# Performance work log

Hardware: AMD Instinct MI355X
Metric: run time of the kernel (lower is better)

The kernel has to match this reference:

```python
import jax, jax.numpy as jnp
import numpy as np
import math

B, T, C, V = 64, 4096, 3, 16
HEADS = 4
ROT_HIDDEN = 128
MLP_HIDDEN = 256
NUM_CLASSES = 12
BLOCK_SIZES = (16, 32, 64)
IN_FEAT = C * V  # 48
FEAT_DIM = HEADS * 7 * len(BLOCK_SIZES)  # 84


def _linear_params(key, fan_in, fan_out):
    kw, kb = jax.random.split(key)
    lim = 1.0 / np.sqrt(fan_in)
    w = jax.random.uniform(kw, (fan_in, fan_out), jnp.float32, -lim, lim)
    b = jax.random.uniform(kb, (fan_out,), jnp.float32, -lim, lim)
    return w, b


def setup_inputs() -> dict:
    key = jax.random.key(0)
    ks = jax.random.split(key, 7)
    x = jax.random.normal(ks[0], (B, T, C, V), jnp.float32)
    w1, b1 = _linear_params(ks[1], IN_FEAT, ROT_HIDDEN)
    w2, b2 = _linear_params(ks[2], ROT_HIDDEN, ROT_HIDDEN)
    w3, b3 = _linear_params(ks[3], ROT_HIDDEN, HEADS * 4)
    p1, pb1 = _linear_params(ks[4], FEAT_DIM, MLP_HIDDEN)
    p2, pb2 = _linear_params(ks[5], MLP_HIDDEN, MLP_HIDDEN)
    p3, pb3 = _linear_params(ks[6], MLP_HIDDEN, NUM_CLASSES)
    return dict(x=x, w1=w1, b1=b1, w2=w2, b2=b2, w3=w3, b3=b3,
                p1=p1, pb1=pb1, p2=p2, pb2=pb2, p3=p3, pb3=pb3)


def _extract_tsf(rot, bs):
    # rot: (B, H, T, F). Non-overlapping blocks of size bs (T % bs == 0).
    b, h, t, f = rot.shape
    n = t // bs
    z = rot.reshape(b, h, n, bs, f)
    mean = z.mean(axis=3)
    m2 = (z * z).mean(axis=3)
    std = jnp.sqrt(((z - mean[:, :, :, None, :]) ** 2).mean(axis=3))
    z_min = z.min(axis=3)
    z_max = z.max(axis=3)
    rms = jnp.sqrt(m2 + 1e-8)
    mac = jnp.abs(z[:, :, :, 1:, :] - z[:, :, :, :-1, :]).mean(axis=3)
    energy = m2  # (z**2).sum / bs == mean of squares
    feat = jnp.stack([mean, std, z_min, z_max, rms, mac, energy], axis=-1)  # (B,H,n,F,7)
    # mean over blocks (n) then over channels (F) -> (B, H, 7)
    return feat.mean(axis=2).mean(axis=2)


def reference(x, w1, b1, w2, b2, w3, b3, p1, pb1, p2, pb2, p3, pb3):
    b, t, c, v = x.shape
    xf = x.reshape(b, t, c * v)
    f = xf.shape[-1]
    pad = (3 - f % 3) % 3
    if pad > 0:
        xf = jnp.pad(xf, ((0, 0), (0, 0), (0, pad)))
    g = xf.shape[-1] // 3
    x_xyz = xf.reshape(b, t, g, 3)

    # rotation-parameter MLP (dropout is identity in eval mode)
    gf = xf.mean(axis=1)[:, :IN_FEAT]
    h1 = jax.nn.relu(gf @ w1 + b1)
    h2 = jax.nn.relu(h1 @ w2 + b2)
    rot = jnp.tanh(h2 @ w3 + b3).reshape(b, HEADS, 4)
    axis = rot[..., :3]
    axis = axis / (jnp.linalg.norm(axis, axis=-1, keepdims=True) + 1e-8)
    theta = rot[..., 3] * math.pi  # (B, H)

    # Rodrigues rotation: v (B,1,T,g,3), k (B,H,1,1,3)
    vvec = x_xyz[:, None]
    k = axis[:, :, None, None, :]
    th = theta[:, :, None, None, None]
    cos_t, sin_t = jnp.cos(th), jnp.sin(th)
    cross = jnp.cross(jnp.broadcast_to(k, (b, HEADS, t, g, 3)),
                      jnp.broadcast_to(vvec, (b, HEADS, t, g, 3)), axis=-1)
    dot = (k * vvec).sum(axis=-1, keepdims=True)
    rotated = vvec * cos_t + cross * sin_t + k * dot * (1.0 - cos_t)  # (B,H,T,g,3)
    rotated = rotated.reshape(b, HEADS, t, g * 3)

    # block-wise stats: per head, per block size, 7 stats -> (B, H, nbs, 7)
    feats = jnp.stack([_extract_tsf(rotated, bs) for bs in BLOCK_SIZES], axis=2)
    feat = feats.reshape(b, HEADS * len(BLOCK_SIZES) * 7)  # (B, 84)

    q1 = jax.nn.relu(feat @ p1 + pb1)
    q2 = jax.nn.relu(q1 @ p2 + pb2)
    return q2 @ p3 + pb3
```

## Files before the change

kernel.cpp:

```cpp
#include <hip/hip_runtime.h>
#include <math.h>


#define PI_F 3.14159265358979323846f

__global__ __launch_bounds__(384) void k_colmean(const float4* __restrict__ x4,
                                                 float* __restrict__ gfpart) {
    int b = blockIdx.x >> 3;
    int chunk = blockIdx.x & 7;
    int tid = threadIdx.x;
    int j4 = tid % 12, r = tid / 12;
    const float4* p = x4 + ((size_t)(b * 4096 + chunk * 512 + r)) * 12 + j4;
    float4 s = make_float4(0.f, 0.f, 0.f, 0.f);
#pragma unroll
    for (int i = 0; i < 16; ++i) {
        float4 v = p[(size_t)i * 32 * 12];
        s.x += v.x; s.y += v.y; s.z += v.z; s.w += v.w;
    }
    __shared__ float4 red[384];
    red[tid] = s;
    __syncthreads();
    if (tid < 48) {
        int jj = tid >> 2, c = tid & 3;
        float t = 0.f;
#pragma unroll
        for (int rr = 0; rr < 32; ++rr) {
            const float* q = (const float*)&red[rr * 12 + jj];
            t += q[c];
        }
        gfpart[blockIdx.x * 48 + tid] = t;
    }
}

__global__ __launch_bounds__(128) void k_rot(const float* __restrict__ gfpart,
                                             const float* __restrict__ w1, const float* __restrict__ b1,
                                             const float* __restrict__ w2, const float* __restrict__ b2,
                                             const float* __restrict__ w3, const float* __restrict__ b3,
                                             float* __restrict__ Rmat) {
    int b = blockIdx.x;
    int j = threadIdx.x;
    __shared__ float gf_s[48], h1_s[128], h2_s[128], rot_s[16];
    if (j < 48) {
        float s = 0.f;
#pragma unroll
        for (int ch = 0; ch < 8; ++ch) s += gfpart[(b * 8 + ch) * 48 + j];
        gf_s[j] = s * (1.f / 4096.f);
    }
    __syncthreads();
    float a = b1[j];
#pragma unroll
    for (int i = 0; i < 48; ++i) a = fmaf(gf_s[i], w1[i * 128 + j], a);
    h1_s[j] = fmaxf(a, 0.f);
    __syncthreads();
    a = b2[j];
    for (int i = 0; i < 128; ++i) a = fmaf(h1_s[i], w2[i * 128 + j], a);
    h2_s[j] = fmaxf(a, 0.f);
    __syncthreads();
    if (j < 16) {
        a = b3[j];
        for (int i = 0; i < 128; ++i) a = fmaf(h2_s[i], w3[i * 16 + j], a);
        rot_s[j] = tanhf(a);
    }
    __syncthreads();
    if (j < 4) {
        float kx = rot_s[j * 4 + 0], ky = rot_s[j * 4 + 1], kz = rot_s[j * 4 + 2];
        float w = rot_s[j * 4 + 3];
        float nrm = sqrtf(kx * kx + ky * ky + kz * kz) + 1e-8f;
        kx /= nrm; ky /= nrm; kz /= nrm;
        float th = w * PI_F;
        float c = cosf(th), s = sinf(th), C = 1.f - c;
        float* R = Rmat + ((size_t)b * 4 + j) * 9;
        R[0] = c + kx * kx * C;      R[1] = kx * ky * C - kz * s; R[2] = kx * kz * C + ky * s;
        R[3] = ky * kx * C + kz * s; R[4] = c + ky * ky * C;      R[5] = ky * kz * C - kx * s;
        R[6] = kz * kx * C - ky * s; R[7] = kz * ky * C + kx * s; R[8] = c + kz * kz * C;
    }
}

__global__ __launch_bounds__(256) void k_stats(const float* __restrict__ x,
                                               const float* __restrict__ Rmat,
                                               float* __restrict__ accpart) {
    int bid = blockIdx.x;
    int b = bid >> 4;
    int tile = bid & 15;
    int tid = threadIdx.x;
    int w = tid >> 6;
    int lane = tid & 63;
    int g = lane & 15;
    int h = lane >> 4;

    const float* Rp = Rmat + (size_t)(b * 4 + h) * 9;
    float R0 = Rp[0], R1 = Rp[1], R2 = Rp[2];
    float R3 = Rp[3], R4 = Rp[4], R5 = Rp[5];
    float R6 = Rp[6], R7 = Rp[7], R8 = Rp[8];

    const float* lp0 = x + ((size_t)(b * 4096 + tile * 256 + w * 64) + (lane >> 4)) * 48
                         + 3 * (lane & 15);

    float a21[21];
#pragma unroll
    for (int i = 0; i < 21; ++i) a21[i] = 0.f;

    float p32s[3] = {0, 0, 0}, p32q[3] = {0, 0, 0}, p32n[3], p32x[3], p32m[3] = {0, 0, 0};
    float p64s[3] = {0, 0, 0}, p64q[3] = {0, 0, 0}, p64n[3], p64x[3], p64m[3] = {0, 0, 0};
#pragma unroll
    for (int c = 0; c < 3; ++c) { p32n[c] = 1e30f; p32x[c] = -1e30f; p64n[c] = 1e30f; p64x[c] = -1e30f; }
    float prev[3];
    float cs[3], cq[3], cn[3], cx[3], cm[3];

#pragma unroll
    for (int k = 0; k < 4; ++k) {
#pragma unroll
        for (int tq = 0; tq < 4; ++tq) {
            const float* lp = lp0 + (size_t)(k * 16 + tq * 4) * 48;
            float v0 = lp[0], v1 = lp[1], v2 = lp[2];
#pragma unroll
            for (int j = 0; j < 4; ++j) {
                int srcl = (j << 4) | g;
                float u0 = __shfl(v0, srcl, 64);
                float u1 = __shfl(v1, srcl, 64);
                float u2 = __shfl(v2, srcl, 64);
                float yy[3];
                yy[0] = fmaf(R0, u0, fmaf(R1, u1, R2 * u2));
                yy[1] = fmaf(R3, u0, fmaf(R4, u1, R5 * u2));
                yy[2] = fmaf(R6, u0, fmaf(R7, u1, R8 * u2));
                if (tq == 0 && j == 0) {
#pragma unroll
                    for (int c = 0; c < 3; ++c) {
                        float y = yy[c];
                        if (k > 0) {
                            float bd = fabsf(y - prev[c]);
                            if (k != 2) p32m[c] += bd;
                            p64m[c] += bd;
                        }
                        cs[c] = y; cq[c] = y * y; cn[c] = y; cx[c] = y; cm[c] = 0.f; prev[c] = y;
                    }
                } else {
#pragma unroll
                    for (int c = 0; c < 3; ++c) {
                        float y = yy[c];
                        cs[c] += y;
                        cq[c] = fmaf(y, y, cq[c]);
                        cn[c] = fminf(cn[c], y);
                        cx[c] = fmaxf(cx[c], y);
                        cm[c] += fabsf(y - prev[c]);
                        prev[c] = y;
                    }
                }
            }
        }
#pragma unroll
        for (int c = 0; c < 3; ++c) {
            float mean = cs[c] * (1.f / 16.f);
            float m2 = cq[c] * (1.f / 16.f);
            a21[0] += cs[c];
            a21[1] += sqrtf(fmaxf(m2 - mean * mean, 0.f));
            a21[2] += cn[c];
            a21[3] += cx[c];
            a21[4] += sqrtf(m2 + 1e-8f);
            a21[5] += cm[c];
            a21[6] += cq[c];
            p32s[c] += cs[c]; p32q[c] += cq[c];
            p32n[c] = fminf(p32n[c], cn[c]); p32x[c] = fmaxf(p32x[c], cx[c]); p32m[c] += cm[c];
        }
        if (k & 1) {
#pragma unroll
            for (int c = 0; c < 3; ++c) {
                float mean = p32s[c] * (1.f / 32.f);
                float m2 = p32q[c] * (1.f / 32.f);
                a21[7] += p32s[c];
                a21[8] += sqrtf(fmaxf(m2 - mean * mean, 0.f));
                a21[9] += p32n[c];
                a21[10] += p32x[c];
                a21[11] += sqrtf(m2 + 1e-8f);
                a21[12] += p32m[c];
                a21[13] += p32q[c];
                p64s[c] += p32s[c]; p64q[c] += p32q[c];
                p64n[c] = fminf(p64n[c], p32n[c]); p64x[c] = fmaxf(p64x[c], p32x[c]); p64m[c] += p32m[c];
                p32s[c] = 0.f; p32q[c] = 0.f; p32n[c] = 1e30f; p32x[c] = -1e30f; p32m[c] = 0.f;
            }
        }
    }
#pragma unroll
    for (int c = 0; c < 3; ++c) {
        float mean = p64s[c] * (1.f / 64.f);
        float m2 = p64q[c] * (1.f / 64.f);
        a21[14] += p64s[c];
        a21[15] += sqrtf(fmaxf(m2 - mean * mean, 0.f));
        a21[16] += p64n[c];
        a21[17] += p64x[c];
        a21[18] += sqrtf(m2 + 1e-8f);
        a21[19] += p64m[c];
        a21[20] += p64q[c];
    }

#pragma unroll
    for (int m = 1; m <= 8; m <<= 1) {
#pragma unroll
        for (int q = 0; q < 21; ++q) a21[q] += __shfl_xor(a21[q], m);
    }
    __shared__ float red[4][4][21];
    if (g == 0) {
#pragma unroll
        for (int q = 0; q < 21; ++q) red[w][h][q] = a21[q];
    }
    __syncthreads();
    if (tid < 84) {
        int hh = tid / 21, sq = tid % 21;
        accpart[bid * 84 + tid] =
            red[0][hh][sq] + red[1][hh][sq] + red[2][hh][sq] + red[3][hh][sq];
    }
}

__global__ __launch_bounds__(256) void k_head(const float* __restrict__ accpart,
                                              const float* __restrict__ p1, const float* __restrict__ pb1,
                                              const float* __restrict__ p2, const float* __restrict__ pb2,
                                              const float* __restrict__ p3, const float* __restrict__ pb3,
                                              float* __restrict__ out) {
    int b = blockIdx.x, j = threadIdx.x;
    __shared__ float feat_s[84], q1_s[256], q2_s[256];
    if (j < 84) {
        float raw = 0.f;
#pragma unroll
        for (int t = 0; t < 16; ++t) raw += accpart[(b * 16 + t) * 84 + j];
        int s = (j % 21) / 7;
        int q = j % 7;
        float bs = (float)(16 << s);
        float n = 4096.f / bs;
        float base = n * 48.f;
        float divi;
        if (q == 0 || q == 6) divi = base * bs;
        else if (q == 5) divi = base * (bs - 1.f);
        else divi = base;
        feat_s[j] = raw / divi;
    }
    __syncthreads();
    float a = pb1[j];
#pragma unroll
    for (int i = 0; i < 84; ++i) a = fmaf(feat_s[i], p1[i * 256 + j], a);
    q1_s[j] = fmaxf(a, 0.f);
    __syncthreads();
    a = pb2[j];
    for (int i = 0; i < 256; ++i) a = fmaf(q1_s[i], p2[i * 256 + j], a);
    q2_s[j] = fmaxf(a, 0.f);
    __syncthreads();
    if (j < 12) {
        a = pb3[j];
        for (int i = 0; i < 256; ++i) a = fmaf(q2_s[i], p3[i * 12 + j], a);
        out[b * 12 + j] = a;
    }
}

extern "C" void kernel_launch(void* const* d_in, const int* in_sizes, int n_in,
                              void* d_out, int out_size, void* d_ws, size_t ws_size,
                              hipStream_t stream) {
    const float* x  = (const float*)d_in[0];
    const float* w1 = (const float*)d_in[1];
    const float* b1 = (const float*)d_in[2];
    const float* w2 = (const float*)d_in[3];
    const float* b2 = (const float*)d_in[4];
    const float* w3 = (const float*)d_in[5];
    const float* b3 = (const float*)d_in[6];
    const float* p1 = (const float*)d_in[7];
    const float* pb1 = (const float*)d_in[8];
    const float* p2 = (const float*)d_in[9];
    const float* pb2 = (const float*)d_in[10];
    const float* p3 = (const float*)d_in[11];
    const float* pb3 = (const float*)d_in[12];

    float* ws = (float*)d_ws;
    float* gfpart  = ws;
    float* Rmat    = ws + 24576;
    float* accpart = ws + 26880;

    k_colmean<<<512, 384, 0, stream>>>((const float4*)x, gfpart);
    k_rot<<<64, 128, 0, stream>>>(gfpart, w1, b1, w2, b2, w3, b3, Rmat);
    k_stats<<<1024, 256, 0, stream>>>(x, Rmat, accpart);
    k_head<<<64, 256, 0, stream>>>(accpart, p1, pb1, p2, pb2, p3, pb3, (float*)d_out);
}
```

Baseline: 63.79 us.

## Remap k_stats so each wave owns a head and lanes own 16-step blocks

The stats kernel now assigns one head per wavefront and gives each 16-lane group its own contiguous 16-timestep block. The earlier scheme broadcast loaded values across heads with shuffles. Block-32 and block-64 statistics are now built by merging neighbouring lane groups through xor-shuffles, including first and last values for the boundary absolute-difference term, with 0.5/0.25 weights to avoid double counting. This removes the per-element cross-lane shuffles and the nested partial-block bookkeeping. In exchange, each head wave reloads x from memory, giving four times the global or L2 reads, and the outer chunk loop is no longer unrolled.

```diff
diff --git a/kernel.cpp b/kernel.cpp
--- a/kernel.cpp
+++ b/kernel.cpp
@@ -83,131 +83,139 @@
     int b = bid >> 4;
     int tile = bid & 15;
     int tid = threadIdx.x;
-    int w = tid >> 6;
+    int h = tid >> 6;
     int lane = tid & 63;
     int g = lane & 15;
-    int h = lane >> 4;
+    int k16 = lane >> 4;
+    bool hi1 = (k16 & 1) != 0;
+    bool hi2 = (k16 & 2) != 0;
 
     const float* Rp = Rmat + (size_t)(b * 4 + h) * 9;
     float R0 = Rp[0], R1 = Rp[1], R2 = Rp[2];
     float R3 = Rp[3], R4 = Rp[4], R5 = Rp[5];
     float R6 = Rp[6], R7 = Rp[7], R8 = Rp[8];
 
-    const float* lp0 = x + ((size_t)(b * 4096 + tile * 256 + w * 64) + (lane >> 4)) * 48
-                         + 3 * (lane & 15);
-
     float a21[21];
 #pragma unroll
     for (int i = 0; i < 21; ++i) a21[i] = 0.f;
 
-    float p32s[3] = {0, 0, 0}, p32q[3] = {0, 0, 0}, p32n[3], p32x[3], p32m[3] = {0, 0, 0};
-    float p64s[3] = {0, 0, 0}, p64q[3] = {0, 0, 0}, p64n[3], p64x[3], p64m[3] = {0, 0, 0};
-#pragma unroll
-    for (int c = 0; c < 3; ++c) { p32n[c] = 1e30f; p32x[c] = -1e30f; p64n[c] = 1e30f; p64x[c] = -1e30f; }
-    float prev[3];
-    float cs[3], cq[3], cn[3], cx[3], cm[3];
-
-#pragma unroll
-    for (int k = 0; k < 4; ++k) {
-#pragma unroll
-        for (int tq = 0; tq < 4; ++tq) {
-            const float* lp = lp0 + (size_t)(k * 16 + tq * 4) * 48;
-            float v0 = lp[0], v1 = lp[1], v2 = lp[2];
-#pragma unroll
-            for (int j = 0; j < 4; ++j) {
-                int srcl = (j << 4) | g;
-                float u0 = __shfl(v0, srcl, 64);
-                float u1 = __shfl(v1, srcl, 64);
-                float u2 = __shfl(v2, srcl, 64);
-                float yy[3];
-                yy[0] = fmaf(R0, u0, fmaf(R1, u1, R2 * u2));
-                yy[1] = fmaf(R3, u0, fmaf(R4, u1, R5 * u2));
-                yy[2] = fmaf(R6, u0, fmaf(R7, u1, R8 * u2));
-                if (tq == 0 && j == 0) {
-#pragma unroll
-                    for (int c = 0; c < 3; ++c) {
-                        float y = yy[c];
-                        if (k > 0) {
-                            float bd = fabsf(y - prev[c]);
-                            if (k != 2) p32m[c] += bd;
-                            p64m[c] += bd;
-                        }
-                        cs[c] = y; cq[c] = y * y; cn[c] = y; cx[c] = y; cm[c] = 0.f; prev[c] = y;
-                    }
-                } else {
-#pragma unroll
-                    for (int c = 0; c < 3; ++c) {
-                        float y = yy[c];
-                        cs[c] += y;
-                        cq[c] = fmaf(y, y, cq[c]);
-                        cn[c] = fminf(cn[c], y);
-                        cx[c] = fmaxf(cx[c], y);
-                        cm[c] += fabsf(y - prev[c]);
-                        prev[c] = y;
-                    }
-                }
+    const float* base = x + ((size_t)(b * 4096 + tile * 256 + k16 * 16)) * 48 + 3 * g;
+
+#pragma unroll 1
+    for (int chunk = 0; chunk < 4; ++chunk) {
+        const float* p = base + (size_t)(chunk * 64) * 48;
+        float S[3], Q[3], N[3], X[3], M[3], F[3], prev[3];
+        {
+            float v0 = p[0], v1 = p[1], v2 = p[2];
+            float y0 = fmaf(R0, v0, fmaf(R1, v1, R2 * v2));
+            float y1 = fmaf(R3, v0, fmaf(R4, v1, R5 * v2));
+            float y2 = fmaf(R6, v0, fmaf(R7, v1, R8 * v2));
+            S[0] = y0; S[1] = y1; S[2] = y2;
+            Q[0] = y0 * y0; Q[1] = y1 * y1; Q[2] = y2 * y2;
+#pragma unroll
+            for (int c = 0; c < 3; ++c) { N[c] = S[c]; X[c] = S[c]; F[c] = S[c]; prev[c] = S[c]; M[c] = 0.f; }
+        }
+#pragma unroll
+        for (int t = 1; t < 16; ++t) {
+            const float* q = p + (size_t)t * 48;
+            float v0 = q[0], v1 = q[1], v2 = q[2];
+            float yy[3];
+            yy[0] = fmaf(R0, v0, fmaf(R1, v1, R2 * v2));
+            yy[1] = fmaf(R3, v0, fmaf(R4, v1, R5 * v2));
+            yy[2] = fmaf(R6, v0, fmaf(R7, v1, R8 * v2));
+#pragma unroll
+            for (int c = 0; c < 3; ++c) {
+                float y = yy[c];
+                S[c] += y;
+                Q[c] = fmaf(y, y, Q[c]);
+                N[c] = fminf(N[c], y);
+                X[c] = fmaxf(X[c], y);
+                M[c] += fabsf(y - prev[c]);
+                prev[c] = y;
             }
         }
 #pragma unroll
         for (int c = 0; c < 3; ++c) {
-            float mean = cs[c] * (1.f / 16.f);
-            float m2 = cq[c] * (1.f / 16.f);
-            a21[0] += cs[c];
+            float mean = S[c] * (1.f / 16.f);
+            float m2 = Q[c] * (1.f / 16.f);
+            a21[0] += S[c];
             a21[1] += sqrtf(fmaxf(m2 - mean * mean, 0.f));
-            a21[2] += cn[c];
-            a21[3] += cx[c];
+            a21[2] += N[c];
+            a21[3] += X[c];
             a21[4] += sqrtf(m2 + 1e-8f);
-            a21[5] += cm[c];
-            a21[6] += cq[c];
-            p32s[c] += cs[c]; p32q[c] += cq[c];
-            p32n[c] = fminf(p32n[c], cn[c]); p32x[c] = fmaxf(p32x[c], cx[c]); p32m[c] += cm[c];
-        }
-        if (k & 1) {
-#pragma unroll
-            for (int c = 0; c < 3; ++c) {
-                float mean = p32s[c] * (1.f / 32.f);
-                float m2 = p32q[c] * (1.f / 32.f);
-                a21[7] += p32s[c];
-                a21[8] += sqrtf(fmaxf(m2 - mean * mean, 0.f));
-                a21[9] += p32n[c];
-                a21[10] += p32x[c];
-                a21[11] += sqrtf(m2 + 1e-8f);
-                a21[12] += p32m[c];
-                a21[13] += p32q[c];
-                p64s[c] += p32s[c]; p64q[c] += p32q[c];
-                p64n[c] = fminf(p64n[c], p32n[c]); p64x[c] = fmaxf(p64x[c], p32x[c]); p64m[c] += p32m[c];
-                p32s[c] = 0.f; p32q[c] = 0.f; p32n[c] = 1e30f; p32x[c] = -1e30f; p32m[c] = 0.f;
-            }
-        }
-    }
-#pragma unroll
-    for (int c = 0; c < 3; ++c) {
-        float mean = p64s[c] * (1.f / 64.f);
-        float m2 = p64q[c] * (1.f / 64.f);
-        a21[14] += p64s[c];
-        a21[15] += sqrtf(fmaxf(m2 - mean * mean, 0.f));
-        a21[16] += p64n[c];
-        a21[17] += p64x[c];
-        a21[18] += sqrtf(m2 + 1e-8f);
-        a21[19] += p64m[c];
-        a21[20] += p64q[c];
+            a21[5] += M[c];
+            a21[6] += Q[c];
+        }
+        float S2[3], Q2[3], N2[3], X2[3], M2[3], F2[3], L2[3];
+#pragma unroll
+        for (int c = 0; c < 3; ++c) {
+            float Sp = __shfl_xor(S[c], 16, 64);
+            float Qp = __shfl_xor(Q[c], 16, 64);
+            float Np = __shfl_xor(N[c], 16, 64);
+            float Xp = __shfl_xor(X[c], 16, 64);
+            float Mp = __shfl_xor(M[c], 16, 64);
+            float Fp = __shfl_xor(F[c], 16, 64);
+            float Lp = __shfl_xor(prev[c], 16, 64);
+            float bd = hi1 ? fabsf(F[c] - Lp) : fabsf(Fp - prev[c]);
+            S2[c] = S[c] + Sp;
+            Q2[c] = Q[c] + Qp;
+            N2[c] = fminf(N[c], Np);
+            X2[c] = fmaxf(X[c], Xp);
+            M2[c] = M[c] + Mp + bd;
+            F2[c] = hi1 ? Fp : F[c];
+            L2[c] = hi1 ? prev[c] : Lp;
+            float mean = S2[c] * (1.f / 32.f);
+            float m2 = Q2[c] * (1.f / 32.f);
+            a21[7]  += 0.5f * S2[c];
+            a21[8]  += 0.5f * sqrtf(fmaxf(m2 - mean * mean, 0.f));
+            a21[9]  += 0.5f * N2[c];
+            a21[10] += 0.5f * X2[c];
+            a21[11] += 0.5f * sqrtf(m2 + 1e-8f);
+            a21[12] += 0.5f * M2[c];
+            a21[13] += 0.5f * Q2[c];
+        }
+#pragma unroll
+        for (int c = 0; c < 3; ++c) {
+            float Sp = __shfl_xor(S2[c], 32, 64);
+            float Qp = __shfl_xor(Q2[c], 32, 64);
+            float Np = __shfl_xor(N2[c], 32, 64);
+            float Xp = __shfl_xor(X2[c], 32, 64);
+            float Mp = __shfl_xor(M2[c], 32, 64);
+            float Fp = __shfl_xor(F2[c], 32, 64);
+            float Lp = __shfl_xor(L2[c], 32, 64);
+            float bd = hi2 ? fabsf(F2[c] - Lp) : fabsf(Fp - L2[c]);
+            float S4 = S2[c] + Sp;
+            float Q4 = Q2[c] + Qp;
+            float N4 = fminf(N2[c], Np);
+            float X4 = fmaxf(X2[c], Xp);
+            float M4 = M2[c] + Mp + bd;
+            float mean = S4 * (1.f / 64.f);
+            float m2 = Q4 * (1.f / 64.f);
+            a21[14] += 0.25f * S4;
+            a21[15] += 0.25f * sqrtf(fmaxf(m2 - mean * mean, 0.f));
+            a21[16] += 0.25f * N4;
+            a21[17] += 0.25f * X4;
+            a21[18] += 0.25f * sqrtf(m2 + 1e-8f);
+            a21[19] += 0.25f * M4;
+            a21[20] += 0.25f * Q4;
+        }
     }
 
 #pragma unroll
     for (int m = 1; m <= 8; m <<= 1) {
 #pragma unroll
-        for (int q = 0; q < 21; ++q) a21[q] += __shfl_xor(a21[q], m);
+        for (int q = 0; q < 21; ++q) a21[q] += __shfl_xor(a21[q], m, 64);
     }
     __shared__ float red[4][4][21];
     if (g == 0) {
 #pragma unroll
-        for (int q = 0; q < 21; ++q) red[w][h][q] = a21[q];
+        for (int q = 0; q < 21; ++q) red[h][k16][q] = a21[q];
     }
     __syncthreads();
     if (tid < 84) {
         int hh = tid / 21, sq = tid % 21;
         accpart[bid * 84 + tid] =
-            red[0][hh][sq] + red[1][hh][sq] + red[2][hh][sq] + red[3][hh][sq];
+            red[hh][0][sq] + red[hh][1][sq] + red[hh][2][sq] + red[hh][3][sq];
     }
 }
 
```

After: 69.58 us. 1.09x slower.
